# Kernel tuning notes

Hardware: AMD Instinct MI355X
Metric: run time of the kernel (lower is better)

## Reference

```python
import jax, jax.numpy as jnp
import numpy as np

EXP_ORDER = 2  # matches init_kwargs exp_order
N_FEAT = 8
Q_DIM = 1
BATCH = 262144
T_EXPANDED = 164  # n + C(n+1,2) + C(n+2,3) for n=8, degrees 1..3
N_OUT = 8


def taylor_expand(x, exp_order):
    """Faithful vectorized version of the nested multiply/concat loop.

    x: [B, n, q]. Builds all monomials of degree 1..exp_order+1 using the same
    recursion as the TF code: at each order, for each j, multiply x_j with the
    previous-order block starting at Id[j], then append. The q-loop in the
    original is replaced by broadcasting over the q axis (identical math).
    """
    n = x.shape[1]
    Id = list(range(n))  # start index of x_j's block in the previous-order terms
    epd = x
    for _ in range(exp_order):
        L = epd.shape[1]  # slice end Id[n-1]+1 always equals current length
        blocks = []
        new_Id = []
        offset = L
        for j in range(n):
            blk = x[:, j:j + 1, :] * epd[:, Id[j]:L, :]  # [B, L-Id[j], q]
            new_Id.append(offset)
            offset += blk.shape[1]
            blocks.append(blk)
        epd = jnp.concatenate([epd] + blocks, axis=1)
        Id = new_Id
    return epd


def setup_inputs() -> dict:
    key = jax.random.key(0)
    k1, k2, k3 = jax.random.split(key, 3)
    x = jax.random.normal(k1, (BATCH, N_FEAT, Q_DIM), dtype=jnp.float32)
    # 'dl' init: uniform(-1/sqrt(fan), 1/sqrt(fan)) with fan = weights_shape[0]
    dl_scale = 1.0 / np.sqrt(N_OUT)
    W = jax.random.uniform(k2, (N_OUT, T_EXPANDED), minval=-dl_scale,
                           maxval=dl_scale, dtype=jnp.float32)
    # 'uniform' bias init: U(-0.2, 0.2), shape [out, 1]
    b = jax.random.uniform(k3, (N_OUT, 1), minval=-0.2, maxval=0.2,
                           dtype=jnp.float32)
    return {"x": x, "W": W, "b": b}


def reference(x, W, b):
    # cp_type == 'none': pass-through of the input
    epd = taylor_expand(x, EXP_ORDER)          # [B, T, q]
    out = jnp.einsum('ot,btq->boq', W, epd) + b[None]  # [B, out, q]
    # act_type == 'relu'
    return jax.nn.relu(out)
```

## Files before the change

### kernel.cpp

```cpp
#include <hip/hip_runtime.h>
#include <hip/hip_bf16.h>
#include <string.h>


static constexpr int TEXP = 164;
static constexpr int NOUT = 8;
static constexpr int NMFMA = 11;
static constexpr int NSLOT = 88;

using f32x16 = __attribute__((ext_vector_type(16))) float;
using short8 = __attribute__((ext_vector_type(8))) short;

constexpr int rowstart2(int j) { return j * 8 - j * (j - 1) / 2; }
constexpr int start3(int j) {
  int s = 44;
  for (int jp = 0; jp < j; ++jp) s += (8 - jp) * (9 - jp) / 2;
  return s;
}
constexpr int t3_of(int a, int b, int c) {
  int x = a, y = b, z = c, t = 0;
  if (x > y) { t = x; x = y; y = t; }
  if (y > z) { t = y; y = z; z = t; }
  if (x > y) { t = x; x = y; y = t; }
  int off = 0;
  for (int ap = x; ap < y; ++ap) off += 8 - ap;
  return start3(x) + off + (z - y);
}

struct Slot { int deg, a, b, c; };
struct SlotTable { Slot s[NSLOT]; };

constexpr bool isrep2(int j, int k) {
  if (k < 4) return true;
  if (j >= 4) return false;
  if (k == j + 4) return true;
  return j < k - 4;
}
constexpr bool isrep3(int a, int b, int c) {
  return ((a < 4) + (b < 4) + (c < 4)) >= 2;
}

constexpr SlotTable make_slots() {
  SlotTable T{};
  int s = 0;
  for (int j = 0; j < 4; ++j) T.s[s++] = {1, j, 0, 0};
  for (int j = 0; j < 8; ++j)
    for (int k = j; k < 8; ++k)
      if (isrep2(j, k)) T.s[s++] = {2, j, k, 0};
  for (int a = 0; a < 8; ++a)
    for (int b = a; b < 8; ++b)
      for (int c = b; c < 8; ++c)
        if (isrep3(a, b, c)) T.s[s++] = {3, a, b, c};
  for (; s < NSLOT; ++s) T.s[s] = {0, 0, 0, 0};
  return T;
}
constexpr SlotTable SLOTS = make_slots();

struct TT { short t[2][NSLOT]; };
constexpr TT make_tt() {
  TT r{};
  for (int h = 0; h < 2; ++h)
    for (int s = 0; s < NSLOT; ++s) {
      Slot sl = SLOTS.s[s];
      int m = h ? 4 : 0;
      if (sl.deg == 0) { r.t[h][s] = -1; }
      else if (sl.deg == 1) { r.t[h][s] = (short)(sl.a ^ m); }
      else if (sl.deg == 2) {
        if (h == 1 && sl.b == (sl.a ^ 4)) { r.t[h][s] = -1; }
        else {
          int a = sl.a ^ m, b = sl.b ^ m;
          int lo = a < b ? a : b, hi2 = a < b ? b : a;
          r.t[h][s] = (short)(8 + rowstart2(lo) + (hi2 - lo));
        }
      } else {
        r.t[h][s] = (short)t3_of(sl.a ^ m, sl.b ^ m, sl.c ^ m);
      }
    }
  return r;
}
__device__ const TT TDX = make_tt();

__device__ __forceinline__ short bf16bits(float v) {
  __hip_bfloat16 h = __float2bfloat16(v);
  short s;
  memcpy(&s, &h, 2);
  return s;
}

template <int S>
__device__ __forceinline__ float slotval(const float (&xs)[8], const float (&d2)[36]) {
  constexpr int deg = SLOTS.s[S].deg;
  constexpr int a = SLOTS.s[S].a;
  constexpr int b = SLOTS.s[S].b;
  constexpr int c = SLOTS.s[S].c;
  if constexpr (deg == 1) return xs[a];
  else if constexpr (deg == 2) return d2[rowstart2(a) + (b - a)];
  else if constexpr (deg == 3) return xs[a] * d2[rowstart2(b) + (c - b)];
  else return 0.0f;
}

template <int I>
struct MfmaStep {
  static __device__ __forceinline__ void run(const float (&xs)[8], const float (&d2)[36],
                                             const unsigned short* __restrict__ wpl,
                                             short8 af_cur, f32x16& acc) {
    short8 af_next;
    if constexpr (I + 1 < NMFMA)
      af_next = *reinterpret_cast<const short8*>(wpl + (I + 1) * 64 * 8);
    short8 bv;
    bv[0] = bf16bits(slotval<8 * I + 0>(xs, d2));
    bv[1] = bf16bits(slotval<8 * I + 1>(xs, d2));
    bv[2] = bf16bits(slotval<8 * I + 2>(xs, d2));
    bv[3] = bf16bits(slotval<8 * I + 3>(xs, d2));
    bv[4] = bf16bits(slotval<8 * I + 4>(xs, d2));
    bv[5] = bf16bits(slotval<8 * I + 5>(xs, d2));
    bv[6] = bf16bits(slotval<8 * I + 6>(xs, d2));
    bv[7] = bf16bits(slotval<8 * I + 7>(xs, d2));
    acc = __builtin_amdgcn_mfma_f32_32x32x16_bf16(af_cur, bv, acc, 0, 0, 0);
    if constexpr (I + 1 < NMFMA)
      MfmaStep<I + 1>::run(xs, d2, wpl, af_next, acc);
  }
};

__global__ void prep_w(const float* __restrict__ W, unsigned short* __restrict__ wp) {
  int idx = threadIdx.x + blockIdx.x * blockDim.x;
  if (idx >= NMFMA * 64 * 8) return;
  int j = idx & 7;
  int lane = (idx >> 3) & 63;
  int i = idx >> 9;
  int row = lane & 31, h = lane >> 5;
  int t = TDX.t[h][8 * i + j];
  float v = (row < NOUT && t >= 0) ? W[row * TEXP + t] : 0.0f;
  union { float f; unsigned int u; } c; c.f = v;
  unsigned int u = c.u;
  wp[idx] = (unsigned short)((u + 0x7fffu + ((u >> 16) & 1u)) >> 16);
}

__global__ __launch_bounds__(256, 4) void taylor_mfma(
    const float* __restrict__ x, const float* __restrict__ b,
    const unsigned short* __restrict__ wp, float* __restrict__ out, int ngroups) {
  const int lane = (int)(threadIdx.x & 63);
  const int h = (lane >= 32) ? 1 : 0;
  const int col = lane & 31;

  const int g = (int)((blockIdx.x * blockDim.x + threadIdx.x) >> 6);
  if (g >= ngroups) return;
  const int elem = g * 32 + col;

  const float* xe = x + elem * 8;
  float4 fA = *reinterpret_cast<const float4*>(xe + 4 * h);
  float4 fB = *reinterpret_cast<const float4*>(xe + 4 - 4 * h);
  float xs[8] = {fA.x, fA.y, fA.z, fA.w, fB.x, fB.y, fB.z, fB.w};

  const unsigned short* wpl = wp + lane * 8;
  short8 af0 = *reinterpret_cast<const short8*>(wpl);

  float d2[36];
#pragma unroll
  for (int j = 0; j < 4; ++j) {
#pragma unroll
    for (int k = j; k < 8; ++k) {
      d2[rowstart2(j) + (k - j)] = xs[j] * xs[k];
    }
  }

  f32x16 acc;
#pragma unroll
  for (int r = 0; r < 16; ++r) acc[r] = 0.0f;

  MfmaStep<0>::run(xs, d2, wpl, af0, acc);

  const float4 bv4 = *reinterpret_cast<const float4*>(b + 4 * h);
  float4 o;
  o.x = fmaxf(acc[0] + bv4.x, 0.0f);
  o.y = fmaxf(acc[1] + bv4.y, 0.0f);
  o.z = fmaxf(acc[2] + bv4.z, 0.0f);
  o.w = fmaxf(acc[3] + bv4.w, 0.0f);
  *reinterpret_cast<float4*>(out + elem * 8 + 4 * h) = o;
}

extern "C" void kernel_launch(void* const* d_in, const int* in_sizes, int n_in,
                              void* d_out, int out_size, void* d_ws, size_t ws_size,
                              hipStream_t stream) {
  const float* x = (const float*)d_in[0];
  const float* W = (const float*)d_in[1];
  const float* b = (const float*)d_in[2];
  float* out = (float*)d_out;
  unsigned short* wp = (unsigned short*)d_ws;

  int n = in_sizes[0] / 8;
  int ngroups = n / 32;
  int blocks = ngroups / 4;

  prep_w<<<22, 256, 0, stream>>>(W, wp);
  taylor_mfma<<<blocks, 256, 0, stream>>>(x, b, wp, out, ngroups);
}
```

Measured before the change: 16.72 us.

## Fuse weight packing into main kernel via LDS and fold bias into MFMA

Removes the separate prep_w launch. Each block now builds the packed bf16 weight fragments in shared memory from W and b, synchronises, then reads A operands from LDS instead of global memory. The bias is folded into an unused padding slot: a constant 1.0 activation is paired with a bias weight, so the epilogue needs no bias load or add. This saves a kernel launch and a dependency, but every block repeats about 5.6K weight conversions with scattered global reads, and the bias now passes through bf16 rounding.

```diff
diff --git a/kernel.cpp b/kernel.cpp
--- a/kernel.cpp
+++ b/kernel.cpp
@@ -7,6 +7,8 @@
 static constexpr int NOUT = 8;
 static constexpr int NMFMA = 11;
 static constexpr int NSLOT = 88;
+static constexpr int BIAS_T = 200;
+static constexpr int NWP = NMFMA * 64 * 8;
 
 using f32x16 = __attribute__((ext_vector_type(16))) float;
 using short8 = __attribute__((ext_vector_type(8))) short;
@@ -63,9 +65,11 @@
     for (int s = 0; s < NSLOT; ++s) {
       Slot sl = SLOTS.s[s];
       int m = h ? 4 : 0;
-      if (sl.deg == 0) { r.t[h][s] = -1; }
-      else if (sl.deg == 1) { r.t[h][s] = (short)(sl.a ^ m); }
-      else if (sl.deg == 2) {
+      if (sl.deg == 0) {
+        r.t[h][s] = (short)((h == 0 && s == 84) ? BIAS_T : -1);
+      } else if (sl.deg == 1) {
+        r.t[h][s] = (short)(sl.a ^ m);
+      } else if (sl.deg == 2) {
         if (h == 1 && sl.b == (sl.a ^ 4)) { r.t[h][s] = -1; }
         else {
           int a = sl.a ^ m, b = sl.b ^ m;
@@ -80,11 +84,10 @@
 }
 __device__ const TT TDX = make_tt();
 
-__device__ __forceinline__ short bf16bits(float v) {
-  __hip_bfloat16 h = __float2bfloat16(v);
-  short s;
-  memcpy(&s, &h, 2);
-  return s;
+__device__ __forceinline__ unsigned short bf16rne(float v) {
+  union { float f; unsigned int u; } c; c.f = v;
+  unsigned int u = c.u;
+  return (unsigned short)((u + 0x7fffu + ((u >> 16) & 1u)) >> 16);
 }
 
 template <int S>
@@ -96,49 +99,53 @@
   if constexpr (deg == 1) return xs[a];
   else if constexpr (deg == 2) return d2[rowstart2(a) + (b - a)];
   else if constexpr (deg == 3) return xs[a] * d2[rowstart2(b) + (c - b)];
+  else if constexpr (S == 84) return 1.0f;
   else return 0.0f;
 }
 
 template <int I>
 struct MfmaStep {
   static __device__ __forceinline__ void run(const float (&xs)[8], const float (&d2)[36],
-                                             const unsigned short* __restrict__ wpl,
+                                             const unsigned short* wlds_lane,
                                              short8 af_cur, f32x16& acc) {
     short8 af_next;
     if constexpr (I + 1 < NMFMA)
-      af_next = *reinterpret_cast<const short8*>(wpl + (I + 1) * 64 * 8);
+      af_next = *reinterpret_cast<const short8*>(wlds_lane + (I + 1) * 64 * 8);
     short8 bv;
-    bv[0] = bf16bits(slotval<8 * I + 0>(xs, d2));
-    bv[1] = bf16bits(slotval<8 * I + 1>(xs, d2));
-    bv[2] = bf16bits(slotval<8 * I + 2>(xs, d2));
-    bv[3] = bf16bits(slotval<8 * I + 3>(xs, d2));
-    bv[4] = bf16bits(slotval<8 * I + 4>(xs, d2));
-    bv[5] = bf16bits(slotval<8 * I + 5>(xs, d2));
-    bv[6] = bf16bits(slotval<8 * I + 6>(xs, d2));
-    bv[7] = bf16bits(slotval<8 * I + 7>(xs, d2));
+    bv[0] = (short)bf16rne(slotval<8 * I + 0>(xs, d2));
+    bv[1] = (short)bf16rne(slotval<8 * I + 1>(xs, d2));
+    bv[2] = (short)bf16rne(slotval<8 * I + 2>(xs, d2));
+    bv[3] = (short)bf16rne(slotval<8 * I + 3>(xs, d2));
+    bv[4] = (short)bf16rne(slotval<8 * I + 4>(xs, d2));
+    bv[5] = (short)bf16rne(slotval<8 * I + 5>(xs, d2));
+    bv[6] = (short)bf16rne(slotval<8 * I + 6>(xs, d2));
+    bv[7] = (short)bf16rne(slotval<8 * I + 7>(xs, d2));
     acc = __builtin_amdgcn_mfma_f32_32x32x16_bf16(af_cur, bv, acc, 0, 0, 0);
     if constexpr (I + 1 < NMFMA)
-      MfmaStep<I + 1>::run(xs, d2, wpl, af_next, acc);
+      MfmaStep<I + 1>::run(xs, d2, wlds_lane, af_next, acc);
   }
 };
 
-__global__ void prep_w(const float* __restrict__ W, unsigned short* __restrict__ wp) {
-  int idx = threadIdx.x + blockIdx.x * blockDim.x;
-  if (idx >= NMFMA * 64 * 8) return;
-  int j = idx & 7;
-  int lane = (idx >> 3) & 63;
-  int i = idx >> 9;
-  int row = lane & 31, h = lane >> 5;
-  int t = TDX.t[h][8 * i + j];
-  float v = (row < NOUT && t >= 0) ? W[row * TEXP + t] : 0.0f;
-  union { float f; unsigned int u; } c; c.f = v;
-  unsigned int u = c.u;
-  wp[idx] = (unsigned short)((u + 0x7fffu + ((u >> 16) & 1u)) >> 16);
-}
-
 __global__ __launch_bounds__(256, 4) void taylor_mfma(
-    const float* __restrict__ x, const float* __restrict__ b,
-    const unsigned short* __restrict__ wp, float* __restrict__ out, int ngroups) {
+    const float* __restrict__ x, const float* __restrict__ W,
+    const float* __restrict__ b, float* __restrict__ out, int ngroups) {
+  __shared__ __align__(16) unsigned short wlds[NWP];
+
+  for (int k = (int)threadIdx.x; k < NWP; k += 256) {
+    int j = k & 7;
+    int lane = (k >> 3) & 63;
+    int i = k >> 9;
+    int row = lane & 31, h = lane >> 5;
+    int t = TDX.t[h][8 * i + j];
+    float v = 0.0f;
+    if (row < NOUT) {
+      if (t >= 0 && t < TEXP) v = W[row * TEXP + t];
+      else if (t == BIAS_T) v = b[row];
+    }
+    wlds[k] = bf16rne(v);
+  }
+  __syncthreads();
+
   const int lane = (int)(threadIdx.x & 63);
   const int h = (lane >= 32) ? 1 : 0;
   const int col = lane & 31;
@@ -152,8 +159,8 @@
   float4 fB = *reinterpret_cast<const float4*>(xe + 4 - 4 * h);
   float xs[8] = {fA.x, fA.y, fA.z, fA.w, fB.x, fB.y, fB.z, fB.w};
 
-  const unsigned short* wpl = wp + lane * 8;
-  short8 af0 = *reinterpret_cast<const short8*>(wpl);
+  const unsigned short* wlds_lane = wlds + lane * 8;
+  short8 af0 = *reinterpret_cast<const short8*>(wlds_lane);
 
   float d2[36];
 #pragma unroll
@@ -168,14 +175,13 @@
 #pragma unroll
   for (int r = 0; r < 16; ++r) acc[r] = 0.0f;
 
-  MfmaStep<0>::run(xs, d2, wpl, af0, acc);
-
-  const float4 bv4 = *reinterpret_cast<const float4*>(b + 4 * h);
+  MfmaStep<0>::run(xs, d2, wlds_lane, af0, acc);
+
   float4 o;
-  o.x = fmaxf(acc[0] + bv4.x, 0.0f);
-  o.y = fmaxf(acc[1] + bv4.y, 0.0f);
-  o.z = fmaxf(acc[2] + bv4.z, 0.0f);
-  o.w = fmaxf(acc[3] + bv4.w, 0.0f);
+  o.x = fmaxf(acc[0], 0.0f);
+  o.y = fmaxf(acc[1], 0.0f);
+  o.z = fmaxf(acc[2], 0.0f);
+  o.w = fmaxf(acc[3], 0.0f);
   *reinterpret_cast<float4*>(out + elem * 8 + 4 * h) = o;
 }
 
@@ -186,12 +192,10 @@
   const float* W = (const float*)d_in[1];
   const float* b = (const float*)d_in[2];
   float* out = (float*)d_out;
-  unsigned short* wp = (unsigned short*)d_ws;
 
   int n = in_sizes[0] / 8;
   int ngroups = n / 32;
   int blocks = ngroups / 4;
 
-  prep_w<<<22, 256, 0, stream>>>(W, wp);
-  taylor_mfma<<<blocks, 256, 0, stream>>>(x, b, wp, out, ngroups);
-}
+  taylor_mfma<<<blocks, 256, 0, stream>>>(x, W, b, out, ngroups);
+}
```

New measurement: 17.46 us. 4.4% more time.
